# Performance work log

Hardware: AMD Instinct MI355X
Metric: run time of the kernel (lower is better)

## Reference

```python
import jax, jax.numpy as jnp
import numpy as np

B, C, H, W = 4, 512, 64, 64
IC = C // 2  # inter_plane
EPS = 1e-5


def _conv1x1(x, w, b=None):
    # x: [b,c,h,w], w: [o,c] -> [b,o,h,w]
    y = jnp.einsum('bchw,oc->bohw', x, w)
    if b is not None:
        y = y + b[None, :, None, None]
    return y


def setup_inputs() -> dict:
    key = jax.random.key(0)
    ks = jax.random.split(key, 20)
    rn = lambda i, sh, s=0.02: jax.random.normal(ks[i], sh, jnp.float32) * s
    return {
        'xA': jax.random.normal(ks[0], (B, C, H, W), jnp.float32),
        'wk': rn(1, (IC, C)), 'bk': rn(2, (IC,)),
        'wv': rn(3, (IC, C)), 'bv': rn(4, (IC,)),
        'wq': rn(5, (IC, C)), 'bq': rn(6, (IC,)),
        'wwg': rn(7, (IC, IC)),
        'bn1_g': jnp.ones((IC,), jnp.float32), 'bn1_b': rn(8, (IC,)),
        'bn1_m': rn(9, (IC,)), 'bn1_v': jax.random.uniform(ks[10], (IC,), jnp.float32, 0.5, 1.5),
        'wout': rn(11, (C, IC)), 'bout': rn(12, (C,)),
        'bn2_g': jnp.ones((C,), jnp.float32), 'bn2_b': rn(13, (C,)),
        'bn2_m': rn(14, (C,)), 'bn2_v': jax.random.uniform(ks[15], (C,), jnp.float32, 0.5, 1.5),
    }


def reference(xA, wk, bk, wv, bv, wq, bq, wwg, bn1_g, bn1_b, bn1_m, bn1_v,
              wout, bout, bn2_g, bn2_b, bn2_m, bn2_v):
    b, c, h, w = xA.shape
    n = h * w
    k = _conv1x1(xA, wk, bk).reshape(b, IC, n)   # [b,ic,n]
    v = _conv1x1(xA, wv, bv).reshape(b, IC, n)   # [b,ic,n] (permuted via einsum below)
    q = _conv1x1(xA, wq, bq).reshape(b, IC, n)   # [b,ic,n]
    # AV = softmax(v^T @ q, axis=2): [b,n,n]
    attn = jax.nn.softmax(jnp.einsum('bcn,bcm->bnm', v, q), axis=2)
    av = jnp.einsum('bcn,bnm->bcm', k, attn)     # [b,ic,n]
    # conv1d 1x1 (no bias) + BatchNorm1d (eval mode)
    avw = jnp.einsum('oc,bcn->bon', wwg, av)
    scale1 = bn1_g / jnp.sqrt(bn1_v + EPS)
    avw = (avw - bn1_m[None, :, None]) * scale1[None, :, None] + bn1_b[None, :, None]
    avw = avw.reshape(b, IC, h, w)
    # out conv + BatchNorm2d (eval) + residual + relu
    o = _conv1x1(avw, wout, bout)
    scale2 = bn2_g / jnp.sqrt(bn2_v + EPS)
    o = (o - bn2_m[None, :, None, None]) * scale2[None, :, None, None] + bn2_b[None, :, None, None]
    return jax.nn.relu(o + xA)
```

## Files before the change

### kernel.cpp

```cpp
#include <hip/hip_runtime.h>


#define N_ 4096
#define C_ 512
#define IC_ 256
#define B_ 4

typedef __bf16 bf16_t;
typedef __bf16 bf16x8 __attribute__((ext_vector_type(8)));
typedef __bf16 bf16x4 __attribute__((ext_vector_type(4)));
typedef float f32x4 __attribute__((ext_vector_type(4)));

#define GLD(g, l) __builtin_amdgcn_global_load_lds(                              \
    (const __attribute__((address_space(1))) void*)(g),                          \
    (__attribute__((address_space(3))) void*)(l), 16, 0, 0)

__device__ __forceinline__ void gemm_bt_128x128(
    const bf16_t* __restrict__ A, int lda,
    const bf16_t* __restrict__ Bt, int ldb,
    int K, int kt0, int m0, int n0,
    bf16_t* lsA, bf16_t* lsB, f32x4 acc[4][4])
{
    const int tid  = threadIdx.x;
    const int wave = tid >> 6, lane = tid & 63;
    const int wr = (wave >> 1) * 64, wc = (wave & 1) * 64;
    const int q = lane >> 4, l15 = lane & 15;
    const int srow = lane >> 3;
    const int scol = (((lane & 7) ^ (srow & 7)) * 8);
    const int swz  = l15 & 7;

    for (int kt = kt0; kt < kt0 + K; kt += 64) {
#pragma unroll
        for (int c = 0; c < 4; ++c) {
            const int ch = wave * 4 + c;
            GLD(A  + (size_t)(m0 + ch * 8 + srow) * lda + kt + scol, lsA + ch * 512);
            GLD(Bt + (size_t)(n0 + ch * 8 + srow) * ldb + kt + scol, lsB + ch * 512);
        }
        __syncthreads();
#pragma unroll
        for (int ks = 0; ks < 2; ++ks) {
            bf16x8 af[4], bfr[4];
            const int co = ((ks * 4 + q) ^ swz) * 8;
#pragma unroll
            for (int i = 0; i < 4; ++i) {
                af[i]  = *(const bf16x8*)&lsA[(wr + i * 16 + l15) * 64 + co];
                bfr[i] = *(const bf16x8*)&lsB[(wc + i * 16 + l15) * 64 + co];
            }
#pragma unroll
            for (int i = 0; i < 4; ++i)
#pragma unroll
                for (int j = 0; j < 4; ++j)
                    acc[i][j] = __builtin_amdgcn_mfma_f32_16x16x32_bf16(
                        af[i], bfr[j], acc[i][j], 0, 0, 0);
        }
        __syncthreads();
    }
}

#define ACC_ZERO(acc)                                                           \
    _Pragma("unroll") for (int i = 0; i < 4; ++i)                               \
    _Pragma("unroll") for (int j = 0; j < 4; ++j)                               \
        acc[i][j] = f32x4{0.f, 0.f, 0.f, 0.f};

__global__ __launch_bounds__(256) void prep_k(
    const float* __restrict__ wk, const float* __restrict__ wv,
    const float* __restrict__ wq,
    const float* __restrict__ wwg, const float* __restrict__ wout,
    const float* __restrict__ bout,
    const float* __restrict__ g1, const float* __restrict__ b1,
    const float* __restrict__ m1, const float* __restrict__ v1,
    const float* __restrict__ g2, const float* __restrict__ b2,
    const float* __restrict__ m2, const float* __restrict__ v2,
    bf16_t* __restrict__ Wb3, bf16_t* __restrict__ Wfb,
    float* __restrict__ bfv, float* __restrict__ rowsum)
{
    const int bid = blockIdx.x;
    __shared__ float ws[256];
    __shared__ float red[4];

    if (bid < 1536) {
        const int i = bid * 256 + threadIdx.x;
        float v;
        if      (i < 131072) v = wk[i];
        else if (i < 262144) v = wv[i - 131072];
        else                 v = wq[i - 262144];
        Wb3[i] = (bf16_t)v;
    } else if (bid < 2048) {
        const int o = bid - 1536;
        const int j = threadIdx.x;
        const float s1 = g1[j] * rsqrtf(v1[j] + 1e-5f);
        const float wo = wout[o * 256 + j];
        ws[j] = wo * s1;
        float bp = wo * (b1[j] - m1[j] * s1);
#pragma unroll
        for (int off = 32; off > 0; off >>= 1) bp += __shfl_down(bp, off);
        if ((j & 63) == 0) red[j >> 6] = bp;
        __syncthreads();

        float acc = 0.f;
#pragma unroll 4
        for (int ic = 0; ic < 256; ++ic)
            acc += ws[ic] * wwg[ic * 256 + j];

        const float s2 = g2[o] * rsqrtf(v2[o] + 1e-5f);
        Wfb[o * 256 + j] = (bf16_t)(acc * s2);
        if (j == 0)
            bfv[o] = s2 * (red[0] + red[1] + red[2] + red[3] + bout[o])
                     - s2 * m2[o] + b2[o];
    } else {
        rowsum[(bid - 2048) * 256 + threadIdx.x] = 0.f;
    }
}

__global__ __launch_bounds__(256) void txa_k(
    const float* __restrict__ xA, bf16_t* __restrict__ xAt)
{
    __shared__ float t[32][33];
    const int b = blockIdx.z;
    const int n0 = blockIdx.x * 32, c0 = blockIdx.y * 32;
    const int tx = threadIdx.x, ty = threadIdx.y;
    const float* X = xA + (size_t)b * C_ * N_;
    bf16_t* Y = xAt + (size_t)b * N_ * C_;
#pragma unroll
    for (int r = 0; r < 4; ++r)
        t[ty + r * 8][tx] = X[(size_t)(c0 + ty + r * 8) * N_ + n0 + tx];
    __syncthreads();
#pragma unroll
    for (int r = 0; r < 4; ++r)
        Y[(size_t)(n0 + ty + r * 8) * C_ + c0 + tx] = (bf16_t)t[tx][ty + r * 8];
}

__global__ __launch_bounds__(256) void conv_mfma_k(
    const bf16_t* __restrict__ Wb3,
    const float* __restrict__ bk, const float* __restrict__ bv,
    const float* __restrict__ bq, const bf16_t* __restrict__ xAt,
    bf16_t* __restrict__ Kb, bf16_t* __restrict__ Vt, bf16_t* __restrict__ Qt)
{
    __shared__ bf16_t smem[16384];
    const int which = blockIdx.z % 3, b = blockIdx.z / 3;
    const bf16_t* A = Wb3 + which * 131072;
    const float* bias = (which == 0) ? bk : (which == 1 ? bv : bq);
    const bf16_t* Bt = xAt + (size_t)b * N_ * C_;
    const int n0 = blockIdx.x * 128, m0 = blockIdx.y * 128;

    f32x4 acc[4][4];
    ACC_ZERO(acc);
    gemm_bt_128x128(A, C_, Bt, C_, C_, 0, m0, n0, smem, smem + 8192, acc);

    const int lane = threadIdx.x & 63, wave = threadIdx.x >> 6;
    const int q = lane >> 4, l15 = lane & 15;
    const int wr = (wave >> 1) * 64, wc = (wave & 1) * 64;

    if (which == 0) {
        bf16_t* Y = Kb + (size_t)b * IC_ * N_;
#pragma unroll
        for (int i = 0; i < 4; ++i)
#pragma unroll
            for (int r = 0; r < 4; ++r) {
                const int o = m0 + wr + i * 16 + q * 4 + r;
                const float bo = bias[o];
#pragma unroll
                for (int j = 0; j < 4; ++j)
                    Y[(size_t)o * N_ + n0 + wc + j * 16 + l15] =
                        (bf16_t)(acc[i][j][r] + bo);
            }
    } else {
        bf16_t* Y = ((which == 1) ? Vt : Qt) + (size_t)b * N_ * IC_;
#pragma unroll
        for (int i = 0; i < 4; ++i) {
            const int ob = m0 + wr + i * 16 + q * 4;
            float bo[4];
#pragma unroll
            for (int r = 0; r < 4; ++r) bo[r] = bias[ob + r];
#pragma unroll
            for (int j = 0; j < 4; ++j) {
                const int n = n0 + wc + j * 16 + l15;
                bf16x4 v4;
#pragma unroll
                for (int r = 0; r < 4; ++r) v4[r] = (bf16_t)(acc[i][j][r] + bo[r]);
                *(bf16x4*)&Y[(size_t)n * IC_ + ob] = v4;
            }
        }
    }
}

__global__ __launch_bounds__(256) void s_mfma_t_k(
    const bf16_t* __restrict__ Qt, const bf16_t* __restrict__ Vt,
    bf16_t* __restrict__ Pt, float* __restrict__ rowsum)
{
    __shared__ bf16_t smem[17408];
    const int b  = blockIdx.z;
    const int n0 = blockIdx.x * 128;
    const int m0 = blockIdx.y * 128;
    const size_t NIC = (size_t)N_ * IC_;
    const bf16_t* Qb = Qt + (size_t)b * NIC;
    const bf16_t* Vb = Vt + (size_t)b * NIC;
    bf16_t* Pb = Pt + (size_t)b * N_ * N_;
    float* rs = rowsum + b * N_;

    f32x4 acc[4][4];
    ACC_ZERO(acc);
    gemm_bt_128x128(Qb, IC_, Vb, IC_, IC_, 0, m0, n0, smem, smem + 8192, acc);

    const int tid = threadIdx.x;
    const int lane = tid & 63, wave = tid >> 6;
    const int q = lane >> 4, l15 = lane & 15;
    const int wr = (wave >> 1) * 64, wc = (wave & 1) * 64;

#pragma unroll
    for (int j = 0; j < 4; ++j) {
        float cs = 0.f;
#pragma unroll
        for (int i = 0; i < 4; ++i)
#pragma unroll
            for (int r = 0; r < 4; ++r) {
                const float e = __expf(acc[i][j][r]);
                cs += e;
                smem[(wr + i * 16 + q * 4 + r) * 136 + wc + j * 16 + l15] = (bf16_t)e;
            }
        cs += __shfl_xor(cs, 16);
        cs += __shfl_xor(cs, 32);
        if (q == 0) atomicAdd(&rs[n0 + wc + j * 16 + l15], cs);
    }
    __syncthreads();

    const int rr = tid >> 4;
    const int cc = (tid & 15) * 8;
#pragma unroll
    for (int p = 0; p < 8; ++p) {
        const int mm = rr + p * 16;
        const bf16x8 v = *(const bf16x8*)&smem[mm * 136 + cc];
        *(bf16x8*)&Pb[(size_t)(m0 + mm) * N_ + n0 + cc] = v;
    }
}

__global__ __launch_bounds__(256) void kscale_k(
    bf16_t* __restrict__ Kb, const float* __restrict__ rowsum)
{
    const size_t i8 = ((size_t)blockIdx.x * 256 + threadIdx.x) * 8;
    const int n = (int)(i8 & (N_ - 1));
    const int b = (int)(i8 >> 20);
    const float* rs = rowsum + b * N_;
    bf16x8 v = *(bf16x8*)&Kb[i8];
    const f32x4 r0 = *(const f32x4*)&rs[n];
    const f32x4 r1 = *(const f32x4*)&rs[n + 4];
#pragma unroll
    for (int k = 0; k < 4; ++k) {
        v[k]     = (bf16_t)((float)v[k]     / r0[k]);
        v[4 + k] = (bf16_t)((float)v[4 + k] / r1[k]);
    }
    *(bf16x8*)&Kb[i8] = v;
}

__global__ __launch_bounds__(256) void av_mfma_k(
    const bf16_t* __restrict__ Pt, const bf16_t* __restrict__ Kb,
    bf16_t* __restrict__ avTb)
{
    __shared__ bf16_t smem[36864];
    const int bid = blockIdx.x;
    const int b   = bid & 3;
    const int m0  = (bid >> 2) * 32;
    const size_t NIC = (size_t)N_ * IC_;
    const bf16_t* Pb  = Pt + (size_t)b * N_ * N_ + (size_t)m0 * N_;
    const bf16_t* Kbb = Kb + (size_t)b * NIC;

    const int tid = threadIdx.x;
    const int wave = tid >> 6, lane = tid & 63;
    const int q = lane >> 4, l15 = lane & 15;
    const int srow = lane >> 3;
    const int scol = (((lane & 7) ^ (srow & 7)) * 8);
    const int swz  = l15 & 7;

    f32x4 acc[2][4];
#pragma unroll
    for (int i = 0; i < 2; ++i)
#pragma unroll
        for (int j = 0; j < 4; ++j) acc[i][j] = f32x4{0.f, 0.f, 0.f, 0.f};

    {
        bf16_t* lsA = smem;
        bf16_t* lsB = smem + 2048;
        GLD(Pb + (size_t)(wave * 8 + srow) * N_ + scol, lsA + wave * 512);
#pragma unroll
        for (int c = 0; c < 8; ++c) {
            const int ch = wave * 8 + c;
            GLD(Kbb + (size_t)(ch * 8 + srow) * N_ + scol, lsB + ch * 512);
        }
    }

    for (int it = 0; it < 64; ++it) {
        __syncthreads();
        const int p = it & 1;
        if (it < 63) {
            const int kt = (it + 1) * 64;
            bf16_t* lsA = smem + (p ^ 1) * 18432;
            bf16_t* lsB = lsA + 2048;
            GLD(Pb + (size_t)(wave * 8 + srow) * N_ + kt + scol, lsA + wave * 512);
#pragma unroll
            for (int c = 0; c < 8; ++c) {
                const int ch = wave * 8 + c;
                GLD(Kbb + (size_t)(ch * 8 + srow) * N_ + kt + scol, lsB + ch * 512);
            }
        }
        bf16_t* lsA = smem + p * 18432;
        bf16_t* lsB = lsA + 2048;
#pragma unroll
        for (int ks = 0; ks < 2; ++ks) {
            const int co = ((ks * 4 + q) ^ swz) * 8;
            bf16x8 af[2], bfr[4];
#pragma unroll
            for (int i = 0; i < 2; ++i)
                af[i]  = *(const bf16x8*)&lsA[(i * 16 + l15) * 64 + co];
#pragma unroll
            for (int j = 0; j < 4; ++j)
                bfr[j] = *(const bf16x8*)&lsB[(wave * 64 + j * 16 + l15) * 64 + co];
#pragma unroll
            for (int i = 0; i < 2; ++i)
#pragma unroll
                for (int j = 0; j < 4; ++j)
                    acc[i][j] = __builtin_amdgcn_mfma_f32_16x16x32_bf16(
                        af[i], bfr[j], acc[i][j], 0, 0, 0);
        }
    }
    __syncthreads();

#pragma unroll
    for (int i = 0; i < 2; ++i)
#pragma unroll
        for (int j = 0; j < 4; ++j)
#pragma unroll
            for (int r = 0; r < 4; ++r)
                smem[(i * 16 + q * 4 + r) * 264 + wave * 64 + j * 16 + l15] =
                    (bf16_t)acc[i][j][r];
    __syncthreads();

    bf16_t* Y = avTb + (size_t)b * NIC + (size_t)m0 * IC_;
    const int erow = tid >> 3;
    const int ecol = (tid & 7) * 8;
#pragma unroll
    for (int p = 0; p < 4; ++p) {
        const int col = ecol + p * 64;
        const bf16x8 v = *(const bf16x8*)&smem[erow * 264 + col];
        *(bf16x8*)&Y[(size_t)erow * IC_ + col] = v;
    }
}

__global__ __launch_bounds__(256) void out_mfma_k(
    const bf16_t* __restrict__ Wfb, const float* __restrict__ bfv,
    const bf16_t* __restrict__ avTb,
    const float* __restrict__ xA, float* __restrict__ out)
{
    __shared__ bf16_t smem[16384];
    const int b = blockIdx.z;
    const bf16_t* Bt = avTb + (size_t)b * N_ * IC_;
    const int n0 = blockIdx.x * 128, o0 = blockIdx.y * 128;

    f32x4 acc[4][4];
    ACC_ZERO(acc);
    gemm_bt_128x128(Wfb, IC_, Bt, IC_, IC_, 0, o0, n0, smem, smem + 8192, acc);

    const int lane = threadIdx.x & 63, wave = threadIdx.x >> 6;
    const int q = lane >> 4, l15 = lane & 15;
    const int wr = (wave >> 1) * 64, wc = (wave & 1) * 64;

#pragma unroll
    for (int i = 0; i < 4; ++i)
#pragma unroll
        for (int r = 0; r < 4; ++r) {
            const int o = o0 + wr + i * 16 + q * 4 + r;
            const float bo = bfv[o];
#pragma unroll
            for (int j = 0; j < 4; ++j) {
                const int n = n0 + wc + j * 16 + l15;
                const size_t idx = ((size_t)b * C_ + o) * N_ + n;
                out[idx] = fmaxf(acc[i][j][r] + bo + xA[idx], 0.f);
            }
        }
}

extern "C" void kernel_launch(void* const* d_in, const int* in_sizes, int n_in,
                              void* d_out, int out_size, void* d_ws, size_t ws_size,
                              hipStream_t stream)
{
    const float* xA    = (const float*)d_in[0];
    const float* wk    = (const float*)d_in[1];
    const float* bk    = (const float*)d_in[2];
    const float* wv    = (const float*)d_in[3];
    const float* bv    = (const float*)d_in[4];
    const float* wq    = (const float*)d_in[5];
    const float* bq    = (const float*)d_in[6];
    const float* wwg   = (const float*)d_in[7];
    const float* bn1_g = (const float*)d_in[8];
    const float* bn1_b = (const float*)d_in[9];
    const float* bn1_m = (const float*)d_in[10];
    const float* bn1_v = (const float*)d_in[11];
    const float* wout  = (const float*)d_in[12];
    const float* bout  = (const float*)d_in[13];
    const float* bn2_g = (const float*)d_in[14];
    const float* bn2_b = (const float*)d_in[15];
    const float* bn2_m = (const float*)d_in[16];
    const float* bn2_v = (const float*)d_in[17];
    float* out = (float*)d_out;

    char* p = (char*)d_ws;
    bf16_t* Wb3    = (bf16_t*)p; p += 786432;
    bf16_t* Wfb    = (bf16_t*)p; p += 262144;
    float*  bfv    = (float*)p;  p += 2048;
    bf16_t* xAt    = (bf16_t*)p;
    bf16_t* avTb   = (bf16_t*)p; p += 16777216;
    bf16_t* Kb     = (bf16_t*)p; p += 8388608;
    bf16_t* Vt     = (bf16_t*)p; p += 8388608;
    bf16_t* Qt     = (bf16_t*)p; p += 8388608;
    float*  rowsum = (float*)p;  p += 65536;
    bf16_t* Pt     = (bf16_t*)p; p += 134217728;

    prep_k<<<2112, 256, 0, stream>>>(wk, wv, wq, wwg, wout, bout,
                                     bn1_g, bn1_b, bn1_m, bn1_v,
                                     bn2_g, bn2_b, bn2_m, bn2_v,
                                     Wb3, Wfb, bfv, rowsum);
    txa_k<<<dim3(N_ / 32, C_ / 32, B_), dim3(32, 8), 0, stream>>>(xA, xAt);
    conv_mfma_k<<<dim3(N_ / 128, IC_ / 128, 3 * B_), 256, 0, stream>>>(
        Wb3, bk, bv, bq, xAt, Kb, Vt, Qt);

    s_mfma_t_k<<<dim3(N_ / 128, N_ / 128, B_), 256, 0, stream>>>(
        Qt, Vt, Pt, rowsum);
    kscale_k<<<2048, 256, 0, stream>>>(Kb, rowsum);
    av_mfma_k<<<N_ / 32 * B_, 256, 0, stream>>>(Pt, Kb, avTb);

    out_mfma_k<<<dim3(N_ / 128, C_ / 128, B_), 256, 0, stream>>>(
        Wfb, bfv, avTb, xA, out);
}
```

Before: 312.7 us.

## Load GEMM A-operand fragments directly from global and fuse prep with transpose

Each lane now reads its A-operand MFMA fragments straight from global memory into registers, skipping the LDS staging. Only the B operand still goes through LDS. This applies to the shared 128x128 GEMM helper and to the attention-times-K kernel. It halves LDS footprint and removes the A-side LDS reads, at the cost of strided, less coalesced global loads whose latency is no longer hidden by the LDS double buffer. Separately, the weight-prep kernel and the xA transpose kernel are merged into one launch to save a kernel launch.

```diff
diff --git a/kernel.cpp b/kernel.cpp
--- a/kernel.cpp
+++ b/kernel.cpp
@@ -15,11 +15,11 @@
     (const __attribute__((address_space(1))) void*)(g),                          \
     (__attribute__((address_space(3))) void*)(l), 16, 0, 0)
 
-__device__ __forceinline__ void gemm_bt_128x128(
+__device__ __forceinline__ void gemm_bt_128x128_ad(
     const bf16_t* __restrict__ A, int lda,
     const bf16_t* __restrict__ Bt, int ldb,
     int K, int kt0, int m0, int n0,
-    bf16_t* lsA, bf16_t* lsB, f32x4 acc[4][4])
+    bf16_t* lsB, f32x4 acc[4][4])
 {
     const int tid  = threadIdx.x;
     const int wave = tid >> 6, lane = tid & 63;
@@ -29,29 +29,37 @@
     const int scol = (((lane & 7) ^ (srow & 7)) * 8);
     const int swz  = l15 & 7;
 
+    const bf16_t* Ar[4];
+#pragma unroll
+    for (int i = 0; i < 4; ++i)
+        Ar[i] = A + (size_t)(m0 + wr + i * 16 + l15) * lda + q * 8;
+
     for (int kt = kt0; kt < kt0 + K; kt += 64) {
 #pragma unroll
         for (int c = 0; c < 4; ++c) {
             const int ch = wave * 4 + c;
-            GLD(A  + (size_t)(m0 + ch * 8 + srow) * lda + kt + scol, lsA + ch * 512);
             GLD(Bt + (size_t)(n0 + ch * 8 + srow) * ldb + kt + scol, lsB + ch * 512);
         }
+        bf16x8 af[4][2];
+#pragma unroll
+        for (int i = 0; i < 4; ++i)
+#pragma unroll
+            for (int ks = 0; ks < 2; ++ks)
+                af[i][ks] = *(const bf16x8*)(Ar[i] + kt + ks * 32);
         __syncthreads();
 #pragma unroll
         for (int ks = 0; ks < 2; ++ks) {
-            bf16x8 af[4], bfr[4];
             const int co = ((ks * 4 + q) ^ swz) * 8;
-#pragma unroll
-            for (int i = 0; i < 4; ++i) {
-                af[i]  = *(const bf16x8*)&lsA[(wr + i * 16 + l15) * 64 + co];
-                bfr[i] = *(const bf16x8*)&lsB[(wc + i * 16 + l15) * 64 + co];
-            }
+            bf16x8 bfr[4];
+#pragma unroll
+            for (int j = 0; j < 4; ++j)
+                bfr[j] = *(const bf16x8*)&lsB[(wc + j * 16 + l15) * 64 + co];
 #pragma unroll
             for (int i = 0; i < 4; ++i)
 #pragma unroll
                 for (int j = 0; j < 4; ++j)
                     acc[i][j] = __builtin_amdgcn_mfma_f32_16x16x32_bf16(
-                        af[i], bfr[j], acc[i][j], 0, 0, 0);
+                        af[i][ks], bfr[j], acc[i][j], 0, 0, 0);
         }
         __syncthreads();
     }
@@ -62,7 +70,7 @@
     _Pragma("unroll") for (int j = 0; j < 4; ++j)                               \
         acc[i][j] = f32x4{0.f, 0.f, 0.f, 0.f};
 
-__global__ __launch_bounds__(256) void prep_k(
+__global__ __launch_bounds__(256) void prep_txa_k(
     const float* __restrict__ wk, const float* __restrict__ wv,
     const float* __restrict__ wq,
     const float* __restrict__ wwg, const float* __restrict__ wout,
@@ -71,23 +79,26 @@
     const float* __restrict__ m1, const float* __restrict__ v1,
     const float* __restrict__ g2, const float* __restrict__ b2,
     const float* __restrict__ m2, const float* __restrict__ v2,
+    const float* __restrict__ xA,
     bf16_t* __restrict__ Wb3, bf16_t* __restrict__ Wfb,
-    float* __restrict__ bfv, float* __restrict__ rowsum)
+    float* __restrict__ bfv, float* __restrict__ rowsum,
+    bf16_t* __restrict__ xAt)
 {
     const int bid = blockIdx.x;
-    __shared__ float ws[256];
-    __shared__ float red[4];
+    const int tid = threadIdx.x;
 
     if (bid < 1536) {
-        const int i = bid * 256 + threadIdx.x;
+        const int i = bid * 256 + tid;
         float v;
         if      (i < 131072) v = wk[i];
         else if (i < 262144) v = wv[i - 131072];
         else                 v = wq[i - 262144];
         Wb3[i] = (bf16_t)v;
     } else if (bid < 2048) {
+        __shared__ float ws[256];
+        __shared__ float red[4];
         const int o = bid - 1536;
-        const int j = threadIdx.x;
+        const int j = tid;
         const float s1 = g1[j] * rsqrtf(v1[j] + 1e-5f);
         const float wo = wout[o * 256 + j];
         ws[j] = wo * s1;
@@ -96,38 +107,34 @@
         for (int off = 32; off > 0; off >>= 1) bp += __shfl_down(bp, off);
         if ((j & 63) == 0) red[j >> 6] = bp;
         __syncthreads();
-
         float acc = 0.f;
 #pragma unroll 4
         for (int ic = 0; ic < 256; ++ic)
             acc += ws[ic] * wwg[ic * 256 + j];
-
         const float s2 = g2[o] * rsqrtf(v2[o] + 1e-5f);
         Wfb[o * 256 + j] = (bf16_t)(acc * s2);
         if (j == 0)
             bfv[o] = s2 * (red[0] + red[1] + red[2] + red[3] + bout[o])
                      - s2 * m2[o] + b2[o];
+    } else if (bid < 2112) {
+        rowsum[(bid - 2048) * 256 + tid] = 0.f;
     } else {
-        rowsum[(bid - 2048) * 256 + threadIdx.x] = 0.f;
-    }
-}
-
-__global__ __launch_bounds__(256) void txa_k(
-    const float* __restrict__ xA, bf16_t* __restrict__ xAt)
-{
-    __shared__ float t[32][33];
-    const int b = blockIdx.z;
-    const int n0 = blockIdx.x * 32, c0 = blockIdx.y * 32;
-    const int tx = threadIdx.x, ty = threadIdx.y;
-    const float* X = xA + (size_t)b * C_ * N_;
-    bf16_t* Y = xAt + (size_t)b * N_ * C_;
-#pragma unroll
-    for (int r = 0; r < 4; ++r)
-        t[ty + r * 8][tx] = X[(size_t)(c0 + ty + r * 8) * N_ + n0 + tx];
-    __syncthreads();
-#pragma unroll
-    for (int r = 0; r < 4; ++r)
-        Y[(size_t)(n0 + ty + r * 8) * C_ + c0 + tx] = (bf16_t)t[tx][ty + r * 8];
+        __shared__ float t[32][33];
+        const int bid2 = bid - 2112;
+        const int b = bid2 >> 11;
+        const int tile = bid2 & 2047;
+        const int n0 = (tile & 127) * 32, c0 = (tile >> 7) * 32;
+        const int tx = tid & 31, ty = tid >> 5;
+        const float* X = xA + (size_t)b * C_ * N_;
+        bf16_t* Y = xAt + (size_t)b * N_ * C_;
+#pragma unroll
+        for (int r = 0; r < 4; ++r)
+            t[ty + r * 8][tx] = X[(size_t)(c0 + ty + r * 8) * N_ + n0 + tx];
+        __syncthreads();
+#pragma unroll
+        for (int r = 0; r < 4; ++r)
+            Y[(size_t)(n0 + ty + r * 8) * C_ + c0 + tx] = (bf16_t)t[tx][ty + r * 8];
+    }
 }
 
 __global__ __launch_bounds__(256) void conv_mfma_k(
@@ -136,7 +143,7 @@
     const float* __restrict__ bq, const bf16_t* __restrict__ xAt,
     bf16_t* __restrict__ Kb, bf16_t* __restrict__ Vt, bf16_t* __restrict__ Qt)
 {
-    __shared__ bf16_t smem[16384];
+    __shared__ bf16_t smem[8192];
     const int which = blockIdx.z % 3, b = blockIdx.z / 3;
     const bf16_t* A = Wb3 + which * 131072;
     const float* bias = (which == 0) ? bk : (which == 1 ? bv : bq);
@@ -145,7 +152,7 @@
 
     f32x4 acc[4][4];
     ACC_ZERO(acc);
-    gemm_bt_128x128(A, C_, Bt, C_, C_, 0, m0, n0, smem, smem + 8192, acc);
+    gemm_bt_128x128_ad(A, C_, Bt, C_, C_, 0, m0, n0, smem, acc);
 
     const int lane = threadIdx.x & 63, wave = threadIdx.x >> 6;
     const int q = lane >> 4, l15 = lane & 15;
@@ -200,7 +207,7 @@
 
     f32x4 acc[4][4];
     ACC_ZERO(acc);
-    gemm_bt_128x128(Qb, IC_, Vb, IC_, IC_, 0, m0, n0, smem, smem + 8192, acc);
+    gemm_bt_128x128_ad(Qb, IC_, Vb, IC_, IC_, 0, m0, n0, smem, acc);
 
     const int tid = threadIdx.x;
     const int lane = tid & 63, wave = tid >> 6;
@@ -256,12 +263,12 @@
     const bf16_t* __restrict__ Pt, const bf16_t* __restrict__ Kb,
     bf16_t* __restrict__ avTb)
 {
-    __shared__ bf16_t smem[36864];
+    __shared__ bf16_t smem[32768];
     const int bid = blockIdx.x;
     const int b   = bid & 3;
     const int m0  = (bid >> 2) * 32;
     const size_t NIC = (size_t)N_ * IC_;
-    const bf16_t* Pb  = Pt + (size_t)b * N_ * N_ + (size_t)m0 * N_;
+    const bf16_t* Pb  = Pt + (size_t)b * N_ * N_;
     const bf16_t* Kbb = Kb + (size_t)b * NIC;
 
     const int tid = threadIdx.x;
@@ -271,46 +278,46 @@
     const int scol = (((lane & 7) ^ (srow & 7)) * 8);
     const int swz  = l15 & 7;
 
+    const bf16_t* Ar[2];
+#pragma unroll
+    for (int i = 0; i < 2; ++i)
+        Ar[i] = Pb + (size_t)(m0 + i * 16 + l15) * N_ + q * 8;
+
     f32x4 acc[2][4];
 #pragma unroll
     for (int i = 0; i < 2; ++i)
 #pragma unroll
         for (int j = 0; j < 4; ++j) acc[i][j] = f32x4{0.f, 0.f, 0.f, 0.f};
 
-    {
-        bf16_t* lsA = smem;
-        bf16_t* lsB = smem + 2048;
-        GLD(Pb + (size_t)(wave * 8 + srow) * N_ + scol, lsA + wave * 512);
-#pragma unroll
-        for (int c = 0; c < 8; ++c) {
-            const int ch = wave * 8 + c;
-            GLD(Kbb + (size_t)(ch * 8 + srow) * N_ + scol, lsB + ch * 512);
-        }
+#pragma unroll
+    for (int c = 0; c < 8; ++c) {
+        const int ch = wave * 8 + c;
+        GLD(Kbb + (size_t)(ch * 8 + srow) * N_ + scol, smem + ch * 512);
     }
 
     for (int it = 0; it < 64; ++it) {
+        const int kt = it * 64;
+        const int p  = it & 1;
+        bf16x8 af[2][2];
+#pragma unroll
+        for (int i = 0; i < 2; ++i)
+#pragma unroll
+            for (int ks = 0; ks < 2; ++ks)
+                af[i][ks] = *(const bf16x8*)(Ar[i] + kt + ks * 32);
         __syncthreads();
-        const int p = it & 1;
         if (it < 63) {
-            const int kt = (it + 1) * 64;
-            bf16_t* lsA = smem + (p ^ 1) * 18432;
-            bf16_t* lsB = lsA + 2048;
-            GLD(Pb + (size_t)(wave * 8 + srow) * N_ + kt + scol, lsA + wave * 512);
+            bf16_t* nb = smem + (p ^ 1) * 16384;
 #pragma unroll
             for (int c = 0; c < 8; ++c) {
                 const int ch = wave * 8 + c;
-                GLD(Kbb + (size_t)(ch * 8 + srow) * N_ + kt + scol, lsB + ch * 512);
+                GLD(Kbb + (size_t)(ch * 8 + srow) * N_ + kt + 64 + scol, nb + ch * 512);
             }
         }
-        bf16_t* lsA = smem + p * 18432;
-        bf16_t* lsB = lsA + 2048;
+        const bf16_t* lsB = smem + p * 16384;
 #pragma unroll
         for (int ks = 0; ks < 2; ++ks) {
             const int co = ((ks * 4 + q) ^ swz) * 8;
-            bf16x8 af[2], bfr[4];
-#pragma unroll
-            for (int i = 0; i < 2; ++i)
-                af[i]  = *(const bf16x8*)&lsA[(i * 16 + l15) * 64 + co];
+            bf16x8 bfr[4];
 #pragma unroll
             for (int j = 0; j < 4; ++j)
                 bfr[j] = *(const bf16x8*)&lsB[(wave * 64 + j * 16 + l15) * 64 + co];
@@ -319,7 +326,7 @@
 #pragma unroll
                 for (int j = 0; j < 4; ++j)
                     acc[i][j] = __builtin_amdgcn_mfma_f32_16x16x32_bf16(
-                        af[i], bfr[j], acc[i][j], 0, 0, 0);
+                        af[i][ks], bfr[j], acc[i][j], 0, 0, 0);
         }
     }
     __syncthreads();
@@ -350,14 +357,14 @@
     const bf16_t* __restrict__ avTb,
     const float* __restrict__ xA, float* __restrict__ out)
 {
-    __shared__ bf16_t smem[16384];
+    __shared__ bf16_t smem[8192];
     const int b = blockIdx.z;
     const bf16_t* Bt = avTb + (size_t)b * N_ * IC_;
     const int n0 = blockIdx.x * 128, o0 = blockIdx.y * 128;
 
     f32x4 acc[4][4];
     ACC_ZERO(acc);
-    gemm_bt_128x128(Wfb, IC_, Bt, IC_, IC_, 0, o0, n0, smem, smem + 8192, acc);
+    gemm_bt_128x128_ad(Wfb, IC_, Bt, IC_, IC_, 0, o0, n0, smem, acc);
 
     const int lane = threadIdx.x & 63, wave = threadIdx.x >> 6;
     const int q = lane >> 4, l15 = lane & 15;
@@ -414,11 +421,10 @@
     float*  rowsum = (float*)p;  p += 65536;
     bf16_t* Pt     = (bf16_t*)p; p += 134217728;
 
-    prep_k<<<2112, 256, 0, stream>>>(wk, wv, wq, wwg, wout, bout,
-                                     bn1_g, bn1_b, bn1_m, bn1_v,
-                                     bn2_g, bn2_b, bn2_m, bn2_v,
-                                     Wb3, Wfb, bfv, rowsum);
-    txa_k<<<dim3(N_ / 32, C_ / 32, B_), dim3(32, 8), 0, stream>>>(xA, xAt);
+    prep_txa_k<<<10304, 256, 0, stream>>>(
+        wk, wv, wq, wwg, wout, bout,
+        bn1_g, bn1_b, bn1_m, bn1_v, bn2_g, bn2_b, bn2_m, bn2_v,
+        xA, Wb3, Wfb, bfv, rowsum, xAt);
     conv_mfma_k<<<dim3(N_ / 128, IC_ / 128, 3 * B_), 256, 0, stream>>>(
         Wb3, bk, bv, bq, xAt, Kb, Vt, Qt);
 
```

New measurement: 371.1 us. 1.19x slower.

## Widen score GEMM tile to 128x256 and merge transpose into prep kernel

Applied to the files above, without the earlier changes.

The score kernel now computes a 128x256 tile per block with an inlined K-loop and 4x8 MFMA accumulators per wave, which halves the block count and raises reuse of the Q tile loaded into LDS. The xA transpose kernel is folded into the prep kernel as extra blocks, removing one launch. The costs are higher register pressure from 128 accumulator floats per lane and a larger LDS footprint of about 66 KB, both of which may lower occupancy.

```diff
diff --git a/kernel.cpp b/kernel.cpp
--- a/kernel.cpp
+++ b/kernel.cpp
@@ -62,7 +62,7 @@
     _Pragma("unroll") for (int j = 0; j < 4; ++j)                               \
         acc[i][j] = f32x4{0.f, 0.f, 0.f, 0.f};
 
-__global__ __launch_bounds__(256) void prep_k(
+__global__ __launch_bounds__(256) void prep_txa_k(
     const float* __restrict__ wk, const float* __restrict__ wv,
     const float* __restrict__ wq,
     const float* __restrict__ wwg, const float* __restrict__ wout,
@@ -71,23 +71,26 @@
     const float* __restrict__ m1, const float* __restrict__ v1,
     const float* __restrict__ g2, const float* __restrict__ b2,
     const float* __restrict__ m2, const float* __restrict__ v2,
+    const float* __restrict__ xA,
     bf16_t* __restrict__ Wb3, bf16_t* __restrict__ Wfb,
-    float* __restrict__ bfv, float* __restrict__ rowsum)
+    float* __restrict__ bfv, float* __restrict__ rowsum,
+    bf16_t* __restrict__ xAt)
 {
     const int bid = blockIdx.x;
-    __shared__ float ws[256];
-    __shared__ float red[4];
+    const int tid = threadIdx.x;
 
     if (bid < 1536) {
-        const int i = bid * 256 + threadIdx.x;
+        const int i = bid * 256 + tid;
         float v;
         if      (i < 131072) v = wk[i];
         else if (i < 262144) v = wv[i - 131072];
         else                 v = wq[i - 262144];
         Wb3[i] = (bf16_t)v;
     } else if (bid < 2048) {
+        __shared__ float ws[256];
+        __shared__ float red[4];
         const int o = bid - 1536;
-        const int j = threadIdx.x;
+        const int j = tid;
         const float s1 = g1[j] * rsqrtf(v1[j] + 1e-5f);
         const float wo = wout[o * 256 + j];
         ws[j] = wo * s1;
@@ -96,38 +99,34 @@
         for (int off = 32; off > 0; off >>= 1) bp += __shfl_down(bp, off);
         if ((j & 63) == 0) red[j >> 6] = bp;
         __syncthreads();
-
         float acc = 0.f;
 #pragma unroll 4
         for (int ic = 0; ic < 256; ++ic)
             acc += ws[ic] * wwg[ic * 256 + j];
-
         const float s2 = g2[o] * rsqrtf(v2[o] + 1e-5f);
         Wfb[o * 256 + j] = (bf16_t)(acc * s2);
         if (j == 0)
             bfv[o] = s2 * (red[0] + red[1] + red[2] + red[3] + bout[o])
                      - s2 * m2[o] + b2[o];
+    } else if (bid < 2112) {
+        rowsum[(bid - 2048) * 256 + tid] = 0.f;
     } else {
-        rowsum[(bid - 2048) * 256 + threadIdx.x] = 0.f;
-    }
-}
-
-__global__ __launch_bounds__(256) void txa_k(
-    const float* __restrict__ xA, bf16_t* __restrict__ xAt)
-{
-    __shared__ float t[32][33];
-    const int b = blockIdx.z;
-    const int n0 = blockIdx.x * 32, c0 = blockIdx.y * 32;
-    const int tx = threadIdx.x, ty = threadIdx.y;
-    const float* X = xA + (size_t)b * C_ * N_;
-    bf16_t* Y = xAt + (size_t)b * N_ * C_;
-#pragma unroll
-    for (int r = 0; r < 4; ++r)
-        t[ty + r * 8][tx] = X[(size_t)(c0 + ty + r * 8) * N_ + n0 + tx];
-    __syncthreads();
-#pragma unroll
-    for (int r = 0; r < 4; ++r)
-        Y[(size_t)(n0 + ty + r * 8) * C_ + c0 + tx] = (bf16_t)t[tx][ty + r * 8];
+        __shared__ float t[32][33];
+        const int bid2 = bid - 2112;
+        const int b = bid2 >> 11;
+        const int tile = bid2 & 2047;
+        const int n0 = (tile & 127) * 32, c0 = (tile >> 7) * 32;
+        const int tx = tid & 31, ty = tid >> 5;
+        const float* X = xA + (size_t)b * C_ * N_;
+        bf16_t* Y = xAt + (size_t)b * N_ * C_;
+#pragma unroll
+        for (int r = 0; r < 4; ++r)
+            t[ty + r * 8][tx] = X[(size_t)(c0 + ty + r * 8) * N_ + n0 + tx];
+        __syncthreads();
+#pragma unroll
+        for (int r = 0; r < 4; ++r)
+            Y[(size_t)(n0 + ty + r * 8) * C_ + c0 + tx] = (bf16_t)t[tx][ty + r * 8];
+    }
 }
 
 __global__ __launch_bounds__(256) void conv_mfma_k(
@@ -188,9 +187,9 @@
     const bf16_t* __restrict__ Qt, const bf16_t* __restrict__ Vt,
     bf16_t* __restrict__ Pt, float* __restrict__ rowsum)
 {
-    __shared__ bf16_t smem[17408];
+    __shared__ bf16_t smem[33792];
     const int b  = blockIdx.z;
-    const int n0 = blockIdx.x * 128;
+    const int n0 = blockIdx.x * 256;
     const int m0 = blockIdx.y * 128;
     const size_t NIC = (size_t)N_ * IC_;
     const bf16_t* Qb = Qt + (size_t)b * NIC;
@@ -198,17 +197,58 @@
     bf16_t* Pb = Pt + (size_t)b * N_ * N_;
     float* rs = rowsum + b * N_;
 
-    f32x4 acc[4][4];
-    ACC_ZERO(acc);
-    gemm_bt_128x128(Qb, IC_, Vb, IC_, IC_, 0, m0, n0, smem, smem + 8192, acc);
-
     const int tid = threadIdx.x;
-    const int lane = tid & 63, wave = tid >> 6;
+    const int wave = tid >> 6, lane = tid & 63;
+    const int wm = (wave >> 1) * 64;
+    const int wn = (wave & 1) * 128;
     const int q = lane >> 4, l15 = lane & 15;
-    const int wr = (wave >> 1) * 64, wc = (wave & 1) * 64;
-
-#pragma unroll
-    for (int j = 0; j < 4; ++j) {
+    const int srow = lane >> 3;
+    const int scol = (((lane & 7) ^ (srow & 7)) * 8);
+    const int swz  = l15 & 7;
+
+    bf16_t* lsA = smem;
+    bf16_t* lsB = smem + 8192;
+
+    f32x4 acc[4][8];
+#pragma unroll
+    for (int i = 0; i < 4; ++i)
+#pragma unroll
+        for (int j = 0; j < 8; ++j) acc[i][j] = f32x4{0.f, 0.f, 0.f, 0.f};
+
+    for (int kt = 0; kt < IC_; kt += 64) {
+#pragma unroll
+        for (int c = 0; c < 4; ++c) {
+            const int ch = wave * 4 + c;
+            GLD(Qb + (size_t)(m0 + ch * 8 + srow) * IC_ + kt + scol, lsA + ch * 512);
+        }
+#pragma unroll
+        for (int c = 0; c < 8; ++c) {
+            const int ch = wave * 8 + c;
+            GLD(Vb + (size_t)(n0 + ch * 8 + srow) * IC_ + kt + scol, lsB + ch * 512);
+        }
+        __syncthreads();
+#pragma unroll
+        for (int ks = 0; ks < 2; ++ks) {
+            const int co = ((ks * 4 + q) ^ swz) * 8;
+            bf16x8 af[4], bfr[8];
+#pragma unroll
+            for (int i = 0; i < 4; ++i)
+                af[i] = *(const bf16x8*)&lsA[(wm + i * 16 + l15) * 64 + co];
+#pragma unroll
+            for (int j = 0; j < 8; ++j)
+                bfr[j] = *(const bf16x8*)&lsB[(wn + j * 16 + l15) * 64 + co];
+#pragma unroll
+            for (int i = 0; i < 4; ++i)
+#pragma unroll
+                for (int j = 0; j < 8; ++j)
+                    acc[i][j] = __builtin_amdgcn_mfma_f32_16x16x32_bf16(
+                        af[i], bfr[j], acc[i][j], 0, 0, 0);
+        }
+        __syncthreads();
+    }
+
+#pragma unroll
+    for (int j = 0; j < 8; ++j) {
         float cs = 0.f;
 #pragma unroll
         for (int i = 0; i < 4; ++i)
@@ -216,21 +256,25 @@
             for (int r = 0; r < 4; ++r) {
                 const float e = __expf(acc[i][j][r]);
                 cs += e;
-                smem[(wr + i * 16 + q * 4 + r) * 136 + wc + j * 16 + l15] = (bf16_t)e;
+                smem[(wm + i * 16 + q * 4 + r) * 264 + wn + j * 16 + l15] = (bf16_t)e;
             }
         cs += __shfl_xor(cs, 16);
         cs += __shfl_xor(cs, 32);
-        if (q == 0) atomicAdd(&rs[n0 + wc + j * 16 + l15], cs);
+        if (q == 0) atomicAdd(&rs[n0 + wn + j * 16 + l15], cs);
     }
     __syncthreads();
 
     const int rr = tid >> 4;
-    const int cc = (tid & 15) * 8;
+    const int c8 = (tid & 15) * 8;
 #pragma unroll
     for (int p = 0; p < 8; ++p) {
         const int mm = rr + p * 16;
-        const bf16x8 v = *(const bf16x8*)&smem[mm * 136 + cc];
-        *(bf16x8*)&Pb[(size_t)(m0 + mm) * N_ + n0 + cc] = v;
+#pragma unroll
+        for (int h = 0; h < 2; ++h) {
+            const int col = c8 + h * 128;
+            const bf16x8 v = *(const bf16x8*)&smem[mm * 264 + col];
+            *(bf16x8*)&Pb[(size_t)(m0 + mm) * N_ + n0 + col] = v;
+        }
     }
 }
 
@@ -414,15 +458,14 @@
     float*  rowsum = (float*)p;  p += 65536;
     bf16_t* Pt     = (bf16_t*)p; p += 134217728;
 
-    prep_k<<<2112, 256, 0, stream>>>(wk, wv, wq, wwg, wout, bout,
-                                     bn1_g, bn1_b, bn1_m, bn1_v,
-                                     bn2_g, bn2_b, bn2_m, bn2_v,
-                                     Wb3, Wfb, bfv, rowsum);
-    txa_k<<<dim3(N_ / 32, C_ / 32, B_), dim3(32, 8), 0, stream>>>(xA, xAt);
+    prep_txa_k<<<10304, 256, 0, stream>>>(
+        wk, wv, wq, wwg, wout, bout,
+        bn1_g, bn1_b, bn1_m, bn1_v, bn2_g, bn2_b, bn2_m, bn2_v,
+        xA, Wb3, Wfb, bfv, rowsum, xAt);
     conv_mfma_k<<<dim3(N_ / 128, IC_ / 128, 3 * B_), 256, 0, stream>>>(
         Wb3, bk, bv, bq, xAt, Kb, Vt, Qt);
 
-    s_mfma_t_k<<<dim3(N_ / 128, N_ / 128, B_), 256, 0, stream>>>(
+    s_mfma_t_k<<<dim3(N_ / 256, N_ / 128, B_), 256, 0, stream>>>(
         Qt, Vt, Pt, rowsum);
     kscale_k<<<2048, 256, 0, stream>>>(Kb, rowsum);
     av_mfma_k<<<N_ / 32 * B_, 256, 0, stream>>>(Pt, Kb, avTb);
```

Result: slower. 332.9 us (+6.5%).
